# Kernel optimization log

Hardware: AMD Instinct MI355X
Metric: run time of the kernel (lower is better)

Reference implementation:

```python
import jax, jax.numpy as jnp
import numpy as np

WS = 8         # window size (square)
SHIFT = 4      # shift size
NUM_HEADS = 8

def _layernorm(x, g, b, eps=1e-5):
    m = x.mean(-1, keepdims=True)
    v = ((x - m) ** 2).mean(-1, keepdims=True)
    return (x - m) / jnp.sqrt(v + eps) * g + b

def _rel_index():
    # relative_position_index for num_frames_q = num_frames_kv = 1 (d-term is 0)
    ch = np.arange(WS)
    coords = np.stack(np.meshgrid(ch, ch, indexing='ij'))      # (2, WS, WS)
    flat = coords.reshape(2, -1)                                 # (2, N)
    rel = flat[:, :, None] - flat[:, None, :]                    # (2, N, N)
    idx = (rel[0] + WS - 1) * (2 * WS - 1) + (rel[1] + WS - 1)   # (N, N)
    return jnp.asarray(idx, dtype=jnp.int32)

def setup_inputs() -> dict:
    key = jax.random.key(0)
    ks = jax.random.split(key, 16)
    B, D, H, W, C = 2, 2, 256, 256, 256
    hid = 4 * C
    nW = (H // WS) * (W // WS)
    N = WS * WS
    f = jax.random.normal
    return {
        'x': f(ks[0], (B, D, H, W, C), jnp.float32),
        'mask_matrix': f(ks[1], (nW, N, N), jnp.float32),
        'g1': jnp.ones((C,), jnp.float32),
        'b1': jnp.zeros((C,), jnp.float32),
        'qw': f(ks[2], (C, C), jnp.float32) * 0.02,
        'qb': jnp.zeros((C,), jnp.float32),
        'kvw': f(ks[3], (2 * C, C), jnp.float32) * 0.02,
        'kvb': jnp.zeros((2 * C,), jnp.float32),
        'pw': f(ks[4], (C, C), jnp.float32) * 0.02,
        'pb': jnp.zeros((C,), jnp.float32),
        'bias_table': f(ks[5], ((2 * WS - 1) ** 2, NUM_HEADS), jnp.float32) * 0.02,
        'g2': jnp.ones((C,), jnp.float32),
        'b2': jnp.zeros((C,), jnp.float32),
        'w1': f(ks[6], (hid, C), jnp.float32) * 0.02,
        'bi1': jnp.zeros((hid,), jnp.float32),
        'w2': f(ks[7], (C, hid), jnp.float32) * 0.02,
        'bi2': jnp.zeros((C,), jnp.float32),
    }

def reference(x, mask_matrix, g1, b1, qw, qb, kvw, kvb, pw, pb, bias_table, g2, b2, w1, bi1, w2, bi2):
    B, D, H, W, C = x.shape
    h = NUM_HEADS
    d = C // h
    N = WS * WS
    nH, nWc = H // WS, W // WS
    nwin = nH * nWc

    shortcut = x[:, 0]                       # (B, H, W, C)  (frame 0)
    xn = _layernorm(x, g1, b1)
    xs = jnp.roll(xn, (-SHIFT, -SHIFT), axis=(2, 3))   # cyclic shift

    # window partition: (B, D, H, W, C) -> (B*nwin, D, N, C)
    win = xs.reshape(B, D, nH, WS, nWc, WS, C)
    win = win.transpose(0, 2, 4, 1, 3, 5, 6).reshape(B * nwin, D, N, C)
    q_in = win[:, 0]                          # (B_, N, C) query = frame 0
    kv_in = win[:, 1]                         # (B_, N, C) kv    = frame 1

    q = (q_in @ qw.T + qb).reshape(-1, N, h, d).transpose(0, 2, 1, 3) * (d ** -0.5)
    kv = (kv_in @ kvw.T + kvb).reshape(-1, N, 2, h, d).transpose(2, 0, 3, 1, 4)
    k, v = kv[0], kv[1]                       # (B_, h, N, d)

    attn = jnp.einsum('bhnd,bhmd->bhnm', q, k)            # (B_, h, N, N)
    bias = bias_table[_rel_index()]                        # (N, N, h)
    attn = attn + bias.transpose(2, 0, 1)[None]
    attn = attn.reshape(B, nwin, h, N, N) + mask_matrix[None, :, None]
    attn = jax.nn.softmax(attn.reshape(-1, h, N, N), axis=-1)

    out = jnp.einsum('bhnm,bhmd->bhnd', attn, v)          # (B_, h, N, d)
    out = out.transpose(0, 2, 1, 3).reshape(-1, N, C)
    out = out @ pw.T + pb + q_in                           # residual inside attn

    # window reverse: (B*nwin, N, C) -> (B, H, W, C)
    out = out.reshape(B, nH, nWc, WS, WS, C).transpose(0, 1, 3, 2, 4, 5).reshape(B, H, W, C)
    out = jnp.roll(out, (SHIFT, SHIFT), axis=(1, 2))

    x1 = shortcut + out
    y = _layernorm(x1, g2, b2)
    y = jax.nn.gelu(y @ w1.T + bi1, approximate=False) @ w2.T + bi2
    return x1 + y
```

## Files before the change

### kernel.cpp

```cpp
#include <hip/hip_runtime.h>
#include <hip/hip_bf16.h>
#include <math.h>

#define SHIFT_ 4

typedef __attribute__((ext_vector_type(8))) short bh8;
typedef __attribute__((ext_vector_type(4))) short sh4;
typedef __attribute__((ext_vector_type(4))) float f4;
typedef __attribute__((ext_vector_type(8))) __bf16 bf8t;

static __device__ __forceinline__ f4 mfma16(bh8 a, bh8 b, f4 c){
  return __builtin_amdgcn_mfma_f32_16x16x32_bf16(
    __builtin_bit_cast(bf8t, a), __builtin_bit_cast(bf8t, b), c, 0, 0, 0);
}
static __device__ __forceinline__ unsigned short f2b(float f){
  unsigned u = __builtin_bit_cast(unsigned, f);
  u += 0x7fffu + ((u >> 16) & 1u);
  return (unsigned short)(u >> 16);
}
static __device__ __forceinline__ float b2f(unsigned short h){
  return __builtin_bit_cast(float, ((unsigned)h) << 16);
}
static __device__ __forceinline__ unsigned cvt_pk_bf16(float lo, float hi){
  unsigned r;
  asm("v_cvt_pk_bf16_f32 %0, %1, %2" : "=v"(r) : "v"(lo), "v"(hi));
  return r;
}
static __device__ __forceinline__ float gelu_f(float hv){
  float u = hv * (1.5957691216f + 0.0713548162f * hv * hv);
  return hv * __builtin_amdgcn_rcpf(1.f + __expf(-u));
}

__global__ __launch_bounds__(256) void prep_w(
    const float* __restrict__ qw, const float* __restrict__ kvw,
    const float* __restrict__ pw, const float* __restrict__ w1,
    const float* __restrict__ w2, unsigned short* __restrict__ wb){
  int i = blockIdx.x * 256 + threadIdx.x;
  float v;
  if      (i < 65536)  v = qw[i] * 0.17677669529663687f;
  else if (i < 196608) v = kvw[i - 65536];
  else if (i < 262144) v = pw[i - 196608];
  else if (i < 524288) v = w1[i - 262144];
  else                 v = w2[i - 524288];
  wb[i] = f2b(v);
}

__global__ __launch_bounds__(256) void ln1_win(
    const float* __restrict__ x, const float* __restrict__ g1,
    const float* __restrict__ b1,
    unsigned short* __restrict__ q_in, unsigned short* __restrict__ kv_in){
  int rid  = blockIdx.x * 4 + (threadIdx.x >> 6);
  int lane = threadIdx.x & 63;
  int d    = rid >> 17;
  int rem  = rid & 131071;
  int w = rem >> 6, n = rem & 63;
  int b = w >> 10, hb = (w >> 5) & 31, wbk = w & 31;
  int sh = (hb * 8 + (n >> 3) + SHIFT_) & 255;
  int sw = (wbk * 8 + (n & 7) + SHIFT_) & 255;
  const float* src = x + ((((size_t)(b * 2 + d)) * 256 + sh) * 256 + sw) * 256;
  float4 v = *(const float4*)(src + lane * 4);
  float s  = v.x + v.y + v.z + v.w;
  float ss = v.x * v.x + v.y * v.y + v.z * v.z + v.w * v.w;
  #pragma unroll
  for (int off = 1; off < 64; off <<= 1){ s += __shfl_xor(s, off); ss += __shfl_xor(ss, off); }
  float m    = s * (1.f / 256.f);
  float rstd = rsqrtf(ss * (1.f / 256.f) - m * m + 1e-5f);
  int c = lane * 4;
  float4 g  = *(const float4*)(g1 + c);
  float4 bb = *(const float4*)(b1 + c);
  sh4 o;
  o.x = (short)f2b((v.x - m) * rstd * g.x + bb.x);
  o.y = (short)f2b((v.y - m) * rstd * g.y + bb.y);
  o.z = (short)f2b((v.z - m) * rstd * g.z + bb.z);
  o.w = (short)f2b((v.w - m) * rstd * g.w + bb.w);
  unsigned short* dst = (d == 0 ? q_in : kv_in) + (size_t)rem * 256 + c;
  *(sh4*)dst = o;
}

template<int MODE, int NT>
__global__ __launch_bounds__(512, 4) void gemm_bt(
    const unsigned short* __restrict__ A, const unsigned short* __restrict__ Wt,
    const float* __restrict__ bias, float bias_scale,
    unsigned short* __restrict__ outb, unsigned short* __restrict__ vpl,
    float* __restrict__ outf, const unsigned short* __restrict__ qin,
    const float* __restrict__ xsrc){
  __shared__ unsigned short sA[128][64];
  __shared__ unsigned short sB[256][64];
  int m0 = blockIdx.x * 128;
  int tid = threadIdx.x, lane = tid & 63, wid = tid >> 6;
  int wm = wid >> 2, wn = wid & 3;
  int llo = lane & 15, lhi = lane >> 4;
  int lr = lane >> 3, lc = (lane & 7) * 8;
  const f4 FZ = {0.f, 0.f, 0.f, 0.f};
  for (int nt = 0; nt < NT; nt++){
    f4 acc[4][4];
    for (int i = 0; i < 4; i++) for (int j = 0; j < 4; j++) acc[i][j] = FZ;
    for (int t = 0; t < 4; t++){
      int k0 = t * 64;
      #pragma unroll
      for (int c = 0; c < 2; c++){
        int rr = wid * 16 + c * 8;
        __builtin_amdgcn_global_load_lds(
          (const __attribute__((address_space(1))) unsigned int*)(A + (size_t)(m0 + rr + lr) * 256 + k0 + lc),
          (__attribute__((address_space(3))) unsigned int*)&sA[rr][0], 16, 0, 0);
      }
      #pragma unroll
      for (int c = 0; c < 4; c++){
        int rb = wid * 32 + c * 8;
        __builtin_amdgcn_global_load_lds(
          (const __attribute__((address_space(1))) unsigned int*)(Wt + (size_t)(nt * 256 + rb + lr) * 256 + k0 + lc),
          (__attribute__((address_space(3))) unsigned int*)&sB[rb][0], 16, 0, 0);
      }
      __syncthreads();
      #pragma unroll
      for (int ks = 0; ks < 2; ks++){
        bh8 a[4], b[4];
        #pragma unroll
        for (int mi = 0; mi < 4; mi++) a[mi] = *(const bh8*)&sA[wm * 64 + mi * 16 + llo][ks * 32 + lhi * 8];
        #pragma unroll
        for (int nj = 0; nj < 4; nj++) b[nj] = *(const bh8*)&sB[wn * 64 + nj * 16 + llo][ks * 32 + lhi * 8];
        #pragma unroll
        for (int mi = 0; mi < 4; mi++)
          #pragma unroll
          for (int nj = 0; nj < 4; nj++){
            if (MODE < 2) acc[mi][nj] = mfma16(b[nj], a[mi], acc[mi][nj]);
            else          acc[mi][nj] = mfma16(a[mi], b[nj], acc[mi][nj]);
          }
      }
      __syncthreads();
    }
    if (MODE < 2){
      #pragma unroll
      for (int nj = 0; nj < 4; nj++){
        int cb = wn * 64 + nj * 16 + lhi * 4;
        int col = nt * 256 + cb;
        float4 bv = *(const float4*)(bias + col);
        #pragma unroll
        for (int mi = 0; mi < 4; mi++){
          int row = m0 + wm * 64 + mi * 16 + llo;
          float f0 = acc[mi][nj][0] + bv.x * bias_scale;
          float f1 = acc[mi][nj][1] + bv.y * bias_scale;
          float f2 = acc[mi][nj][2] + bv.z * bias_scale;
          float f3 = acc[mi][nj][3] + bv.w * bias_scale;
          uint2 p;
          p.x = cvt_pk_bf16(f0, f1);
          p.y = cvt_pk_bf16(f2, f3);
          if (MODE == 0 || nt == 0) *(uint2*)(outb + (size_t)row * 256 + cb) = p;
          else                      *(uint2*)(vpl  + (size_t)row * 256 + cb) = p;
        }
      }
    } else {
      #pragma unroll
      for (int mi = 0; mi < 4; mi++)
        #pragma unroll
        for (int nj = 0; nj < 4; nj++){
          int col = wn * 64 + nj * 16 + llo;
          float bv = bias[col] * bias_scale;
          #pragma unroll
          for (int r = 0; r < 4; r++){
            int row = m0 + wm * 64 + mi * 16 + lhi * 4 + r;
            int w = row >> 6, n = row & 63;
            int b = w >> 10, hb = (w >> 5) & 31, wbk = w & 31;
            int hh = (hb * 8 + (n >> 3) + SHIFT_) & 255;
            int ww = (wbk * 8 + (n & 7) + SHIFT_) & 255;
            float res = b2f(qin[(size_t)row * 256 + col]);
            float sc  = xsrc[((((size_t)(b * 2)) * 256 + hh) * 256 + ww) * 256 + col];
            outf[(((size_t)b * 256 + hh) * 256 + ww) * 256 + col] = acc[mi][nj][r] + bv + res + sc;
          }
        }
    }
  }
}

__global__ __launch_bounds__(64) void attn_k(
    const unsigned short* __restrict__ q, const unsigned short* __restrict__ k,
    const unsigned short* __restrict__ v, const float* __restrict__ mask,
    const float* __restrict__ bias_table, unsigned short* __restrict__ aout){
  __shared__ unsigned short sQ[64][40];
  __shared__ unsigned short sK[64][40];
  __shared__ unsigned short sV[64][34];
  __shared__ unsigned short sVT[32][72];
  __shared__ unsigned short sP[64][72];
  __shared__ float sBias[225];
  int bid = blockIdx.x;
  int w = bid >> 3, hd = bid & 7;
  int lane = threadIdx.x;
  int llo = lane & 15, lhi = lane >> 4;
  for (int i = lane; i < 225; i += 64) sBias[i] = bias_table[i * 8 + hd];
  {
    const unsigned short* qp = q + ((size_t)w * 64 + lane) * 256 + hd * 32;
    const unsigned short* kp = k + ((size_t)w * 64 + lane) * 256 + hd * 32;
    const unsigned short* vp = v + ((size_t)w * 64 + lane) * 256 + hd * 32;
    #pragma unroll
    for (int c2 = 0; c2 < 4; c2++){
      *(bh8*)&sQ[lane][c2 * 8] = *(const bh8*)(qp + c2 * 8);
      *(bh8*)&sK[lane][c2 * 8] = *(const bh8*)(kp + c2 * 8);
      *(bh8*)&sV[lane][c2 * 8] = *(const bh8*)(vp + c2 * 8);
    }
  }
  __syncthreads();
  const f4 FZ = {0.f, 0.f, 0.f, 0.f};
  f4 acc[4][4];
  {
    bh8 a[4], b[4];
    #pragma unroll
    for (int mi = 0; mi < 4; mi++) a[mi] = *(const bh8*)&sQ[mi * 16 + llo][lhi * 8];
    #pragma unroll
    for (int nj = 0; nj < 4; nj++) b[nj] = *(const bh8*)&sK[nj * 16 + llo][lhi * 8];
    #pragma unroll
    for (int mi = 0; mi < 4; mi++)
      #pragma unroll
      for (int nj = 0; nj < 4; nj++)
        acc[mi][nj] = mfma16(a[mi], b[nj], FZ);
  }
  {
    int dv = lane >> 1, n0 = (lane & 1) * 32;
    #pragma unroll
    for (int i = 0; i < 32; i += 2){
      unsigned lo = sV[n0 + i][dv], hi = sV[n0 + i + 1][dv];
      *(unsigned*)&sVT[dv][n0 + i] = lo | (hi << 16);
    }
  }
  const float* mrow = mask + (size_t)(w & 1023) * 4096;
  #pragma unroll
  for (int mi = 0; mi < 4; mi++){
    #pragma unroll
    for (int r = 0; r < 4; r++){
      int rr = mi * 16 + lhi * 4 + r;
      int yi = rr >> 3, xi = rr & 7;
      float sv[4]; float mx = -1e30f;
      #pragma unroll
      for (int nj = 0; nj < 4; nj++){
        int cc = nj * 16 + llo;
        int idx = (yi - (cc >> 3) + 7) * 15 + (xi - (cc & 7) + 7);
        sv[nj] = acc[mi][nj][r] + sBias[idx] + mrow[rr * 64 + cc];
        mx = fmaxf(mx, sv[nj]);
      }
      #pragma unroll
      for (int off = 1; off < 16; off <<= 1) mx = fmaxf(mx, __shfl_xor(mx, off));
      float sum = 0.f;
      #pragma unroll
      for (int nj = 0; nj < 4; nj++){ sv[nj] = __expf(sv[nj] - mx); sum += sv[nj]; }
      #pragma unroll
      for (int off = 1; off < 16; off <<= 1) sum += __shfl_xor(sum, off);
      float inv = __builtin_amdgcn_rcpf(sum);
      #pragma unroll
      for (int nj = 0; nj < 4; nj++) sP[rr][nj * 16 + llo] = f2b(sv[nj] * inv);
    }
  }
  __syncthreads();
  f4 o[4][2];
  for (int mi = 0; mi < 4; mi++) for (int dj = 0; dj < 2; dj++) o[mi][dj] = FZ;
  #pragma unroll
  for (int ks = 0; ks < 2; ks++){
    bh8 pa[4], vb[2];
    #pragma unroll
    for (int mi = 0; mi < 4; mi++) pa[mi] = *(const bh8*)&sP[mi * 16 + llo][ks * 32 + lhi * 8];
    #pragma unroll
    for (int dj = 0; dj < 2; dj++) vb[dj] = *(const bh8*)&sVT[dj * 16 + llo][ks * 32 + lhi * 8];
    #pragma unroll
    for (int mi = 0; mi < 4; mi++)
      #pragma unroll
      for (int dj = 0; dj < 2; dj++)
        o[mi][dj] = mfma16(pa[mi], vb[dj], o[mi][dj]);
  }
  #pragma unroll
  for (int mi = 0; mi < 4; mi++)
    for (int dj = 0; dj < 2; dj++)
      for (int r = 0; r < 4; r++){
        int rr = mi * 16 + lhi * 4 + r, dd = dj * 16 + llo;
        aout[((size_t)w * 64 + rr) * 256 + hd * 32 + dd] = f2b(o[mi][dj][r]);
      }
}

__global__ __launch_bounds__(256) void ln2_k(
    const float* __restrict__ x1, const float* __restrict__ g2,
    const float* __restrict__ b2, unsigned short* __restrict__ xn){
  int rid  = blockIdx.x * 4 + (threadIdx.x >> 6);
  int lane = threadIdx.x & 63;
  const float* xr = x1 + (size_t)rid * 256;
  float4 v = *(const float4*)(xr + lane * 4);
  float s  = v.x + v.y + v.z + v.w;
  float ss = v.x * v.x + v.y * v.y + v.z * v.z + v.w * v.w;
  #pragma unroll
  for (int off = 1; off < 64; off <<= 1){ s += __shfl_xor(s, off); ss += __shfl_xor(ss, off); }
  float m    = s * (1.f / 256.f);
  float rstd = rsqrtf(ss * (1.f / 256.f) - m * m + 1e-5f);
  int c = lane * 4;
  float4 g  = *(const float4*)(g2 + c);
  float4 bb = *(const float4*)(b2 + c);
  sh4 o;
  o.x = (short)f2b((v.x - m) * rstd * g.x + bb.x);
  o.y = (short)f2b((v.y - m) * rstd * g.y + bb.y);
  o.z = (short)f2b((v.z - m) * rstd * g.z + bb.z);
  o.w = (short)f2b((v.w - m) * rstd * g.w + bb.w);
  *(sh4*)(xn + (size_t)rid * 256 + c) = o;
}

template<int KSTEPS, int EPI, int BIASF>
__global__ __launch_bounds__(256, 3) void mlp_gemm(
    const unsigned short* __restrict__ A, int lda,
    const unsigned short* __restrict__ Bw, int ldb,
    const float* __restrict__ bias,
    unsigned short* __restrict__ outb, int ldo,
    float* __restrict__ outf){
  __shared__ unsigned short sA[128][64];
  __shared__ unsigned short sB[128][64];
  int n0 = blockIdx.x * 128, m0 = blockIdx.y * 128;
  int tid = threadIdx.x, lane = tid & 63, wid = tid >> 6;
  int wm = wid >> 1, wn = wid & 1;
  int llo = lane & 15, lhi = lane >> 4;
  int lr = lane >> 3, lc = (lane & 7) * 8;
  const f4 FZ = {0.f, 0.f, 0.f, 0.f};
  f4 acc[4][4];
  for (int i = 0; i < 4; i++) for (int j = 0; j < 4; j++) acc[i][j] = FZ;

  for (int t = 0; t < KSTEPS; t++){
    int k0 = t * 64;
    #pragma unroll
    for (int c = 0; c < 4; c++){
      int rr = wid * 32 + c * 8 + lr;
      __builtin_amdgcn_global_load_lds(
        (const __attribute__((address_space(1))) unsigned int*)(A + (size_t)(m0 + rr) * lda + k0 + lc),
        (__attribute__((address_space(3))) unsigned int*)&sA[wid * 32 + c * 8][0], 16, 0, 0);
      __builtin_amdgcn_global_load_lds(
        (const __attribute__((address_space(1))) unsigned int*)(Bw + (size_t)(n0 + rr) * ldb + k0 + lc),
        (__attribute__((address_space(3))) unsigned int*)&sB[wid * 32 + c * 8][0], 16, 0, 0);
    }
    __syncthreads();
    #pragma unroll
    for (int ks = 0; ks < 2; ks++){
      bh8 a[4], b[4];
      #pragma unroll
      for (int mi = 0; mi < 4; mi++) a[mi] = *(const bh8*)&sA[wm * 64 + mi * 16 + llo][ks * 32 + lhi * 8];
      #pragma unroll
      for (int nj = 0; nj < 4; nj++) b[nj] = *(const bh8*)&sB[wn * 64 + nj * 16 + llo][ks * 32 + lhi * 8];
      #pragma unroll
      for (int mi = 0; mi < 4; mi++)
        #pragma unroll
        for (int nj = 0; nj < 4; nj++){
          if (EPI == 0) acc[mi][nj] = mfma16(b[nj], a[mi], acc[mi][nj]);
          else          acc[mi][nj] = mfma16(a[mi], b[nj], acc[mi][nj]);
        }
    }
    __syncthreads();
  }
  if (EPI == 0){
    #pragma unroll
    for (int nj = 0; nj < 4; nj++){
      int cb = n0 + wn * 64 + nj * 16 + lhi * 4;
      float4 bv = *(const float4*)(bias + cb);
      #pragma unroll
      for (int mi = 0; mi < 4; mi++){
        int row = m0 + wm * 64 + mi * 16 + llo;
        float g0 = gelu_f(acc[mi][nj][0] + bv.x);
        float g1 = gelu_f(acc[mi][nj][1] + bv.y);
        float g2 = gelu_f(acc[mi][nj][2] + bv.z);
        float g3 = gelu_f(acc[mi][nj][3] + bv.w);
        uint2 p;
        p.x = cvt_pk_bf16(g0, g1);
        p.y = cvt_pk_bf16(g2, g3);
        *(uint2*)(outb + (size_t)row * ldo + cb) = p;
      }
    }
  } else {
    #pragma unroll
    for (int mi = 0; mi < 4; mi++)
      #pragma unroll
      for (int nj = 0; nj < 4; nj++){
        int col = n0 + wn * 64 + nj * 16 + llo;
        float bv = BIASF ? bias[col] : 0.f;
        #pragma unroll
        for (int r = 0; r < 4; r++){
          int row = m0 + wm * 64 + mi * 16 + lhi * 4 + r;
          outf[(size_t)row * 256 + col] += acc[mi][nj][r] + bv;
        }
      }
  }
}

extern "C" void kernel_launch(void* const* d_in, const int* in_sizes, int n_in,
                              void* d_out, int out_size, void* d_ws, size_t ws_size,
                              hipStream_t stream){
  const float* x          = (const float*)d_in[0];
  const float* mask       = (const float*)d_in[1];
  const float* g1         = (const float*)d_in[2];
  const float* b1         = (const float*)d_in[3];
  const float* qw         = (const float*)d_in[4];
  const float* qb         = (const float*)d_in[5];
  const float* kvw        = (const float*)d_in[6];
  const float* kvb        = (const float*)d_in[7];
  const float* pw         = (const float*)d_in[8];
  const float* pb         = (const float*)d_in[9];
  const float* bias_table = (const float*)d_in[10];
  const float* g2         = (const float*)d_in[11];
  const float* b2         = (const float*)d_in[12];
  const float* w1         = (const float*)d_in[13];
  const float* bi1        = (const float*)d_in[14];
  const float* w2         = (const float*)d_in[15];
  const float* bi2        = (const float*)d_in[16];
  float* out = (float*)d_out;
  char* ws = (char*)d_ws;
  const long long MB = 1048576LL;
  unsigned short* wb    = (unsigned short*)(ws);
  unsigned short* q_in  = (unsigned short*)(ws + (long long)(1.5 * MB));
  unsigned short* kv_in = (unsigned short*)(ws + (long long)(65.5 * MB));
  unsigned short* qbuf  = (unsigned short*)(ws + (long long)(129.5 * MB));
  unsigned short* kbuf  = (unsigned short*)(ws + (long long)(193.5 * MB));
  unsigned short* vbuf  = (unsigned short*)(ws + (long long)(257.5 * MB));
  unsigned short* aoutb = kv_in;
  unsigned short* xn    = vbuf;
  unsigned short* Hh    = q_in;

  prep_w<<<3072, 256, 0, stream>>>(qw, kvw, pw, w1, w2, wb);
  ln1_win<<<65536, 256, 0, stream>>>(x, g1, b1, q_in, kv_in);
  gemm_bt<0, 1><<<1024, 512, 0, stream>>>(q_in, wb, qb, 0.17677669529663687f,
                                          qbuf, nullptr, nullptr, nullptr, nullptr);
  gemm_bt<1, 2><<<1024, 512, 0, stream>>>(kv_in, wb + 65536, kvb, 1.0f,
                                          kbuf, vbuf, nullptr, nullptr, nullptr);
  attn_k<<<16384, 64, 0, stream>>>(qbuf, kbuf, vbuf, mask, bias_table, aoutb);
  gemm_bt<2, 1><<<1024, 512, 0, stream>>>(aoutb, wb + 196608, pb, 1.0f,
                                          nullptr, nullptr, out, q_in, x);
  ln2_k<<<32768, 256, 0, stream>>>(out, g2, b2, xn);
  const unsigned short* w1b = wb + 262144;
  const unsigned short* w2b = wb + 524288;
  for (int h = 0; h < 2; h++){
    const long long R = (long long)h * 65536;
    mlp_gemm<4, 0, 0><<<dim3(8, 512), 256, 0, stream>>>(xn + R * 256, 256, w1b, 256,
                                                        bi1, Hh, 1024, nullptr);
    mlp_gemm<16, 1, 1><<<dim3(2, 512), 256, 0, stream>>>(Hh, 1024, w2b, 1024,
                                                         bi2, nullptr, 0, out + R * 256);
  }
}
```

Baseline: 829.1 us.

## Process four heads per attention block sharing a bf16 mask tile in LDS

Restructures the window attention kernel so each 256-thread block handles four heads of one window, with one wave per head. The fp32 mask row is loaded once per block, converted to bf16 and shared in LDS instead of being re-read from global memory by every head. Q and K fragments now load straight from global memory into registers, and V is transposed directly into LDS, removing the intermediate staging copies. Storing the mask as bf16 loses some precision in the softmax logits, and the larger LDS footprint may limit how many blocks fit per CU.

```diff
diff --git a/kernel.cpp b/kernel.cpp
--- a/kernel.cpp
+++ b/kernel.cpp
@@ -172,56 +172,58 @@
   }
 }
 
-__global__ __launch_bounds__(64) void attn_k(
+__global__ __launch_bounds__(256, 2) void attn_k(
     const unsigned short* __restrict__ q, const unsigned short* __restrict__ k,
     const unsigned short* __restrict__ v, const float* __restrict__ mask,
     const float* __restrict__ bias_table, unsigned short* __restrict__ aout){
-  __shared__ unsigned short sQ[64][40];
-  __shared__ unsigned short sK[64][40];
-  __shared__ unsigned short sV[64][34];
-  __shared__ unsigned short sVT[32][72];
-  __shared__ unsigned short sP[64][72];
-  __shared__ float sBias[225];
+  __shared__ unsigned short sMask[64][72];
+  __shared__ unsigned short sVT[128][72];
+  __shared__ unsigned short sP[4][64][72];
+  __shared__ float sBias[4][225];
   int bid = blockIdx.x;
-  int w = bid >> 3, hd = bid & 7;
-  int lane = threadIdx.x;
+  int w = bid >> 1, hg = bid & 1;
+  int tid = threadIdx.x, lane = tid & 63, wid = tid >> 6;
+  int hd = hg * 4 + wid;
   int llo = lane & 15, lhi = lane >> 4;
-  for (int i = lane; i < 225; i += 64) sBias[i] = bias_table[i * 8 + hd];
+  const unsigned short* qp = q + (size_t)w * 64 * 256 + hd * 32;
+  const unsigned short* kp = k + (size_t)w * 64 * 256 + hd * 32;
+  bh8 af[4], bf[4];
+  #pragma unroll
+  for (int mi = 0; mi < 4; mi++) af[mi] = *(const bh8*)(qp + (size_t)(mi * 16 + llo) * 256 + lhi * 8);
+  #pragma unroll
+  for (int nj = 0; nj < 4; nj++) bf[nj] = *(const bh8*)(kp + (size_t)(nj * 16 + llo) * 256 + lhi * 8);
+  const float* mrow = mask + (size_t)(w & 1023) * 4096;
+  #pragma unroll
+  for (int i = 0; i < 2; i++){
+    int base = (tid + i * 256) * 8;
+    float4 u0 = *(const float4*)(mrow + base);
+    float4 u1 = *(const float4*)(mrow + base + 4);
+    int rr = base >> 6, cc = base & 63;
+    uint4 p;
+    p.x = cvt_pk_bf16(u0.x, u0.y); p.y = cvt_pk_bf16(u0.z, u0.w);
+    p.z = cvt_pk_bf16(u1.x, u1.y); p.w = cvt_pk_bf16(u1.z, u1.w);
+    *(uint4*)&sMask[rr][cc] = p;
+  }
   {
-    const unsigned short* qp = q + ((size_t)w * 64 + lane) * 256 + hd * 32;
-    const unsigned short* kp = k + ((size_t)w * 64 + lane) * 256 + hd * 32;
-    const unsigned short* vp = v + ((size_t)w * 64 + lane) * 256 + hd * 32;
-    #pragma unroll
-    for (int c2 = 0; c2 < 4; c2++){
-      *(bh8*)&sQ[lane][c2 * 8] = *(const bh8*)(qp + c2 * 8);
-      *(bh8*)&sK[lane][c2 * 8] = *(const bh8*)(kp + c2 * 8);
-      *(bh8*)&sV[lane][c2 * 8] = *(const bh8*)(vp + c2 * 8);
-    }
-  }
-  __syncthreads();
+    const unsigned short* vp = v + (size_t)w * 64 * 256 + hg * 128;
+    #pragma unroll
+    for (int it = 0; it < 4; it++){
+      int idx = tid + it * 256;
+      int n = idx >> 4, dc = (idx & 15) * 8;
+      bh8 vv = *(const bh8*)(vp + (size_t)n * 256 + dc);
+      #pragma unroll
+      for (int j = 0; j < 8; j++) sVT[dc + j][n] = (unsigned short)vv[j];
+    }
+  }
+  for (int i = lane; i < 225; i += 64) sBias[wid][i] = bias_table[i * 8 + hd];
   const f4 FZ = {0.f, 0.f, 0.f, 0.f};
   f4 acc[4][4];
-  {
-    bh8 a[4], b[4];
-    #pragma unroll
-    for (int mi = 0; mi < 4; mi++) a[mi] = *(const bh8*)&sQ[mi * 16 + llo][lhi * 8];
-    #pragma unroll
-    for (int nj = 0; nj < 4; nj++) b[nj] = *(const bh8*)&sK[nj * 16 + llo][lhi * 8];
-    #pragma unroll
-    for (int mi = 0; mi < 4; mi++)
-      #pragma unroll
-      for (int nj = 0; nj < 4; nj++)
-        acc[mi][nj] = mfma16(a[mi], b[nj], FZ);
-  }
-  {
-    int dv = lane >> 1, n0 = (lane & 1) * 32;
-    #pragma unroll
-    for (int i = 0; i < 32; i += 2){
-      unsigned lo = sV[n0 + i][dv], hi = sV[n0 + i + 1][dv];
-      *(unsigned*)&sVT[dv][n0 + i] = lo | (hi << 16);
-    }
-  }
-  const float* mrow = mask + (size_t)(w & 1023) * 4096;
+  #pragma unroll
+  for (int mi = 0; mi < 4; mi++)
+    #pragma unroll
+    for (int nj = 0; nj < 4; nj++)
+      acc[mi][nj] = mfma16(af[mi], bf[nj], FZ);
+  __syncthreads();
   #pragma unroll
   for (int mi = 0; mi < 4; mi++){
     #pragma unroll
@@ -233,7 +235,7 @@
       for (int nj = 0; nj < 4; nj++){
         int cc = nj * 16 + llo;
         int idx = (yi - (cc >> 3) + 7) * 15 + (xi - (cc & 7) + 7);
-        sv[nj] = acc[mi][nj][r] + sBias[idx] + mrow[rr * 64 + cc];
+        sv[nj] = acc[mi][nj][r] + sBias[wid][idx] + b2f(sMask[rr][cc]);
         mx = fmaxf(mx, sv[nj]);
       }
       #pragma unroll
@@ -245,19 +247,18 @@
       for (int off = 1; off < 16; off <<= 1) sum += __shfl_xor(sum, off);
       float inv = __builtin_amdgcn_rcpf(sum);
       #pragma unroll
-      for (int nj = 0; nj < 4; nj++) sP[rr][nj * 16 + llo] = f2b(sv[nj] * inv);
-    }
-  }
-  __syncthreads();
+      for (int nj = 0; nj < 4; nj++) sP[wid][rr][nj * 16 + llo] = f2b(sv[nj] * inv);
+    }
+  }
   f4 o[4][2];
   for (int mi = 0; mi < 4; mi++) for (int dj = 0; dj < 2; dj++) o[mi][dj] = FZ;
   #pragma unroll
   for (int ks = 0; ks < 2; ks++){
     bh8 pa[4], vb[2];
     #pragma unroll
-    for (int mi = 0; mi < 4; mi++) pa[mi] = *(const bh8*)&sP[mi * 16 + llo][ks * 32 + lhi * 8];
-    #pragma unroll
-    for (int dj = 0; dj < 2; dj++) vb[dj] = *(const bh8*)&sVT[dj * 16 + llo][ks * 32 + lhi * 8];
+    for (int mi = 0; mi < 4; mi++) pa[mi] = *(const bh8*)&sP[wid][mi * 16 + llo][ks * 32 + lhi * 8];
+    #pragma unroll
+    for (int dj = 0; dj < 2; dj++) vb[dj] = *(const bh8*)&sVT[wid * 32 + dj * 16 + llo][ks * 32 + lhi * 8];
     #pragma unroll
     for (int mi = 0; mi < 4; mi++)
       #pragma unroll
@@ -418,7 +419,7 @@
                                           qbuf, nullptr, nullptr, nullptr, nullptr);
   gemm_bt<1, 2><<<1024, 512, 0, stream>>>(kv_in, wb + 65536, kvb, 1.0f,
                                           kbuf, vbuf, nullptr, nullptr, nullptr);
-  attn_k<<<16384, 64, 0, stream>>>(qbuf, kbuf, vbuf, mask, bias_table, aoutb);
+  attn_k<<<4096, 256, 0, stream>>>(qbuf, kbuf, vbuf, mask, bias_table, aoutb);
   gemm_bt<2, 1><<<1024, 512, 0, stream>>>(aoutb, wb + 196608, pb, 1.0f,
                                           nullptr, nullptr, out, q_in, x);
   ln2_k<<<32768, 256, 0, stream>>>(out, g2, b2, xn);
```

Result: faster. 768.9 us (-7.3%).
